# Performance work log

Hardware: AMD Instinct MI355X
Metric: run time of the kernel (lower is better)

## Reference

```python
import jax, jax.numpy as jnp
import numpy as np

DIM = 64
D_STATE = 64          # = d_inner // 2, required for consistency
D_CONV = 4
EXPAND = 2
D_INNER = EXPAND * DIM  # 128
BATCH = 2
SEQ = 2048


def setup_inputs() -> dict:
    key = jax.random.key(0)
    k0, k1, k2, k3, k4, k5 = jax.random.split(key, 6)
    return {
        "x": jax.random.normal(k0, (BATCH, SEQ, DIM), jnp.float32),
        # torch nn.Linear weight layout: (out_features, in_features)
        "W_proj": jax.random.normal(k1, (3 * D_INNER, DIM), jnp.float32) / np.sqrt(DIM),
        # torch depthwise Conv1d weight layout: (d_inner, 1, d_conv)
        "conv_w": jax.random.normal(k2, (D_INNER, 1, D_CONV), jnp.float32) / np.sqrt(D_CONV),
        "conv_b": jax.random.normal(k3, (D_INNER,), jnp.float32) * 0.01,
        # negative A so exp(delta * rowsum(A)) is a stable decay (<1)
        "A": -jnp.abs(jax.random.normal(k4, (D_STATE, D_STATE), jnp.float32)) * 0.1,
        "D": jax.random.normal(k5, (D_INNER,), jnp.float32),
    }


def _scan_dir(A_bar, bx, reverse):
    # A_bar, bx: (B, L, n, d). Linear recurrence h_t = A_t * h_{t-1} + bx_t.
    A_t = jnp.moveaxis(A_bar, 1, 0)  # (L, B, n, d)
    b_t = jnp.moveaxis(bx, 1, 0)
    h0 = jnp.zeros(A_t.shape[1:], A_t.dtype)

    def step(h, inp):
        a, b = inp
        h = a * h + b
        return h, h

    _, hs = jax.lax.scan(step, h0, (A_t, b_t), reverse=reverse)
    return jnp.moveaxis(hs, 0, 1)  # (B, L, n, d)


def _forward(x, W_proj, conv_w, conv_b, A, D):
    d_inner = D.shape[0]
    n = A.shape[0]
    k = conv_w.shape[-1]

    xp = x @ W_proj.T                                   # (B, L, 3*d_inner)
    x_c_in, delta_raw, BC = jnp.split(xp, [d_inner, 2 * d_inner], axis=-1)

    # causal depthwise conv1d (torch pads d_conv-1 both sides then slices [:L])
    xc = jnp.swapaxes(x_c_in, 1, 2)                     # (B, d, L)
    xc = jax.lax.conv_general_dilated(
        xc, conv_w, window_strides=(1,), padding=[(k - 1, 0)],
        dimension_numbers=("NCH", "OIH", "NCH"), feature_group_count=d_inner)
    xc = xc + conv_b[None, :, None]
    x_conv = jnp.swapaxes(xc, 1, 2)                     # (B, L, d_inner)

    delta = jax.nn.sigmoid(delta_raw)                   # (B, L, d_inner)
    B_in, C_in = BC[..., :n], BC[..., n:]               # (B, L, n) each

    a = A.sum(axis=1)                                   # 'ij->i' contraction, (n,)
    # A_bar[b,l,n,d] = exp(delta[b,l,d] * a[n])
    A_bar = jnp.exp(delta[:, :, None, :] * a[None, None, :, None])
    # (delta*B) * x, broadcast into (B, L, n, d)
    bx = (delta * x_conv)[:, :, None, :] * B_in[..., None]

    h = _scan_dir(A_bar, bx, False) + _scan_dir(A_bar, bx, True)  # (B,L,n,d)

    y = jnp.einsum("blnd,bln->bld", h, C_in) + D * x_conv
    return y


def reference(x, W_proj, conv_w, conv_b, A, D):
    return _forward(x, W_proj, conv_w, conv_b, A, D)
```

## Files before the change

### kernel.cpp

```cpp
#include <hip/hip_runtime.h>

#define BB   2
#define TT   2048
#define DIN  128
#define NS   64
#define CL   16
#define NC   128
#define NSUP 16
#define SUPW 8
#define NP   32
#define L2E  1.4426950408889634f

typedef float f2_t __attribute__((ext_vector_type(2)));
typedef float f4_t __attribute__((ext_vector_type(4)));

#if __has_builtin(__builtin_amdgcn_exp2f)
__device__ __forceinline__ float fexp2(float x) { return __builtin_amdgcn_exp2f(x); }
#else
__device__ __forceinline__ float fexp2(float x) { return exp2f(x); }
#endif

__device__ __forceinline__ unsigned int f2bfu(float f) {
  unsigned int u = __float_as_uint(f);
  u += 0x7FFFu + ((u >> 16) & 1u);
  return u >> 16;
}
__device__ __forceinline__ unsigned int packbf2(float a, float b) {
  return f2bfu(a) | (f2bfu(b) << 16);
}
__device__ __forceinline__ float bflo(unsigned int u) { return __uint_as_float(u << 16); }
__device__ __forceinline__ float bfhi(unsigned int u) { return __uint_as_float(u & 0xFFFF0000u); }

__global__ __launch_bounds__(128) void k_proj(
    const float* __restrict__ x, const float* __restrict__ W,
    const float* __restrict__ A,
    float* __restrict__ xcin, float* __restrict__ delta,
    float* __restrict__ Bb, float* __restrict__ Cb, float* __restrict__ a2g) {
  __shared__ float xs[128 * 65];
  int tile = blockIdx.x, rg = blockIdx.y, tid = threadIdx.x;
  int base = tile * 128;
  const float4* __restrict__ x4 = (const float4*)(x + (size_t)base * 64);
  for (int i = tid; i < 128 * 16; i += 128) {
    float4 v = x4[i];
    int row = i >> 4, c4 = (i & 15) << 2;
    xs[row * 65 + c4 + 0] = v.x;
    xs[row * 65 + c4 + 1] = v.y;
    xs[row * 65 + c4 + 2] = v.z;
    xs[row * 65 + c4 + 3] = v.w;
  }
  if (tile == 0 && rg == 0 && tid < NS) {
    float s = 0.f;
    for (int m = 0; m < NS; ++m) s += A[tid * NS + m];
    a2g[tid] = s * L2E;
  }
  __syncthreads();
  float xr[64];
#pragma unroll
  for (int k = 0; k < 64; ++k) xr[k] = xs[tid * 65 + k];
  int bt = base + tid;
#pragma unroll 4
  for (int rr = 0; rr < 16; ++rr) {
    int r = rg * 16 + rr;
    const float* __restrict__ wrow = W + r * 64;
    float a0 = 0.f, a1 = 0.f, a2 = 0.f, a3 = 0.f;
#pragma unroll
    for (int k = 0; k < 64; k += 4) {
      a0 = fmaf(xr[k + 0], wrow[k + 0], a0);
      a1 = fmaf(xr[k + 1], wrow[k + 1], a1);
      a2 = fmaf(xr[k + 2], wrow[k + 2], a2);
      a3 = fmaf(xr[k + 3], wrow[k + 3], a3);
    }
    float acc = (a0 + a1) + (a2 + a3);
    if (r < 128) {
      xcin[(size_t)bt * DIN + r] = acc;
    } else if (r < 256) {
      delta[(size_t)bt * DIN + (r - 128)] = 1.f / (1.f + fexp2(-acc * L2E));
    } else if (r < 320) {
      Bb[(size_t)bt * NS + (r - 256)] = acc;
    } else {
      Cb[(size_t)bt * NS + (r - 320)] = acc;
    }
  }
}

__global__ __launch_bounds__(1024) void k_scan1(
    const float* __restrict__ xcin, const float* __restrict__ delta,
    const float* __restrict__ Bb, const float* __restrict__ a2g,
    const float* __restrict__ cw, const float* __restrict__ cb,
    unsigned int* __restrict__ hendP, float* __restrict__ sumd) {
  __shared__ float xcs[(CL + 3) * DIN];
  __shared__ float des[CL * DIN];
  __shared__ float Bs[CL * NS];
  int c = blockIdx.x, b = blockIdx.y;
  int tid = threadIdx.x;
  int d = tid & 127;
  int g = __builtin_amdgcn_readfirstlane(tid >> 7);
  int t0 = c * CL;
  {
    const float* __restrict__ xcB = xcin + (size_t)b * TT * DIN;
    for (int i = tid; i < (CL + 3) * 32; i += 1024) {
      int row = i >> 5, c4 = i & 31;
      int t = t0 - 3 + row;
      float4 v = make_float4(0.f, 0.f, 0.f, 0.f);
      if (t >= 0) v = ((const float4*)(xcB + (size_t)t * DIN))[c4];
      ((float4*)xcs)[i] = v;
    }
    if (tid < CL * 32)
      ((float4*)des)[tid] = ((const float4*)(delta + (size_t)(b * TT + t0) * DIN))[tid];
    if (tid < CL * 16)
      ((float4*)Bs)[tid] = ((const float4*)(Bb + (size_t)(b * TT + t0) * NS))[tid];
  }
  float cw0 = cw[d * 4 + 0], cw1 = cw[d * 4 + 1], cw2 = cw[d * 4 + 2], cw3 = cw[d * 4 + 3];
  float cbd = cb[d];
  int nb = g * 8;
  f2_t a2p[4];
#pragma unroll
  for (int j = 0; j < 4; ++j) { a2p[j].x = a2g[nb + 2 * j]; a2p[j].y = a2g[nb + 2 * j + 1]; }
  __syncthreads();
  f2_t hf[4], hr[4], Pp[4];
#pragma unroll
  for (int j = 0; j < 4; ++j) {
    hf[j] = (f2_t){0.f, 0.f}; hr[j] = (f2_t){0.f, 0.f}; Pp[j] = (f2_t){1.f, 1.f};
  }
  float sd = 0.f;
  float w0 = xcs[0 * DIN + d], w1 = xcs[1 * DIN + d], w2 = xcs[2 * DIN + d];
#pragma unroll
  for (int i = 0; i < CL; ++i) {
    float w3 = xcs[(i + 3) * DIN + d];
    float xconv = fmaf(cw0, w0, fmaf(cw1, w1, fmaf(cw2, w2, fmaf(cw3, w3, cbd))));
    float de = des[i * DIN + d];
    sd += de;
    float dxv = de * xconv;
    const f2_t* __restrict__ B2 = (const f2_t*)&Bs[i * NS + nb];
#pragma unroll
    for (int j = 0; j < 4; ++j) {
      f2_t b2 = dxv * B2[j];
      f2_t e2;
      e2.x = fexp2(de * a2p[j].x);
      e2.y = fexp2(de * a2p[j].y);
      hf[j] = e2 * hf[j] + b2;
      hr[j] = Pp[j] * b2 + hr[j];
      Pp[j] = Pp[j] * e2;
    }
    w0 = w1; w1 = w2; w2 = w3;
  }
  size_t h0 = (((size_t)(0 * NC + c) * BB + b) * NP + (nb >> 1)) * DIN + d;
  size_t h1 = (((size_t)(1 * NC + c) * BB + b) * NP + (nb >> 1)) * DIN + d;
#pragma unroll
  for (int j = 0; j < 4; ++j) {
    hendP[h0 + (size_t)j * DIN] = packbf2(hf[j].x, hf[j].y);
    hendP[h1 + (size_t)j * DIN] = packbf2(hr[j].x, hr[j].y);
  }
  if (g == 0) sumd[(c * BB + b) * DIN + d] = sd;
}

__global__ __launch_bounds__(512) void k_comb(
    const unsigned int* __restrict__ hendP, const float* __restrict__ sumd,
    const float* __restrict__ a2g, unsigned int* __restrict__ hinP) {
  __shared__ float S0[NSUP][64], S1[NSUP][64];
  __shared__ float sdS[NSUP][64];
  __shared__ float C0[NSUP][64], C1[NSUP][64];
  int bid = blockIdx.x;
  int dh = bid & 1;
  int np = (bid >> 1) & 31;
  int dir = (bid >> 6) & 1;
  int b = bid >> 7;
  int tid = threadIdx.x;
  int dl = tid & 63;
  int d = dh * 64 + dl;
  int sl = __builtin_amdgcn_readfirstlane(tid >> 6);
  float a2n0 = a2g[2 * np], a2n1 = a2g[2 * np + 1];
  float hinLo0[2][SUPW], hinLo1[2][SUPW], pfLoc[2][SUPW];
#pragma unroll
  for (int ss = 0; ss < 2; ++ss) {
    int sp = sl + ss * 8;
    float c0 = 0.f, c1 = 0.f, pf = 0.f;
#pragma unroll
    for (int k = 0; k < SUPW; ++k) {
      int cc = sp * SUPW + (dir ? (SUPW - 1 - k) : k);
      float sdv = sumd[(cc * BB + b) * DIN + d];
      unsigned int hv = hendP[(((size_t)(dir * NC + cc) * BB + b) * NP + np) * DIN + d];
      hinLo0[ss][k] = c0; hinLo1[ss][k] = c1; pfLoc[ss][k] = pf;
      float e0 = fexp2(a2n0 * sdv);
      float e1 = fexp2(a2n1 * sdv);
      c0 = fmaf(e0, c0, bflo(hv));
      c1 = fmaf(e1, c1, bfhi(hv));
      pf += sdv;
    }
    S0[sp][dl] = c0; S1[sp][dl] = c1; sdS[sp][dl] = pf;
  }
  __syncthreads();
  if (sl == 0) {
    float c0 = 0.f, c1 = 0.f;
#pragma unroll
    for (int k = 0; k < NSUP; ++k) {
      int sp = dir ? (NSUP - 1 - k) : k;
      C0[sp][dl] = c0; C1[sp][dl] = c1;
      float sv = sdS[sp][dl];
      float e0 = fexp2(a2n0 * sv);
      float e1 = fexp2(a2n1 * sv);
      c0 = fmaf(e0, c0, S0[sp][dl]);
      c1 = fmaf(e1, c1, S1[sp][dl]);
    }
  }
  __syncthreads();
#pragma unroll
  for (int ss = 0; ss < 2; ++ss) {
    int sp = sl + ss * 8;
    float cs0 = C0[sp][dl], cs1 = C1[sp][dl];
#pragma unroll
    for (int k = 0; k < SUPW; ++k) {
      int cc = sp * SUPW + (dir ? (SUPW - 1 - k) : k);
      float pe0 = fexp2(a2n0 * pfLoc[ss][k]);
      float pe1 = fexp2(a2n1 * pfLoc[ss][k]);
      float v0 = fmaf(pe0, cs0, hinLo0[ss][k]);
      float v1 = fmaf(pe1, cs1, hinLo1[ss][k]);
      hinP[(((size_t)(dir * NC + cc) * BB + b) * NP + np) * DIN + d] = packbf2(v0, v1);
    }
  }
}

__global__ __launch_bounds__(1024) void k_scan2(
    const float* __restrict__ xcin, const float* __restrict__ delta,
    const float* __restrict__ Bb, const float* __restrict__ Cb,
    const float* __restrict__ a2g, const float* __restrict__ cw,
    const float* __restrict__ cb, const float* __restrict__ Dp,
    const unsigned int* __restrict__ hinP,
    float* __restrict__ out) {
  __shared__ float yred[8][CL][DIN];
  int c = blockIdx.x, b = blockIdx.y;
  int tid = threadIdx.x;
  int d = tid & 127;
  int g = __builtin_amdgcn_readfirstlane(tid >> 7);
  int dir = g >> 2;
  int nb = (g & 3) * 16;
  float cw0 = cw[d * 4 + 0], cw1 = cw[d * 4 + 1], cw2 = cw[d * 4 + 2], cw3 = cw[d * 4 + 3];
  float cbd = cb[d];
  float Dd = Dp[d];
  f2_t a2p[8];
#pragma unroll
  for (int j = 0; j < 8; ++j) { a2p[j].x = a2g[nb + 2 * j]; a2p[j].y = a2g[nb + 2 * j + 1]; }
  f2_t h2[8];
  size_t hb0 = (((size_t)(dir * NC + c) * BB + b) * NP + (nb >> 1)) * DIN + d;
#pragma unroll
  for (int jp = 0; jp < 8; ++jp) {
    unsigned int u = hinP[hb0 + (size_t)jp * DIN];
    h2[jp].x = bflo(u);
    h2[jp].y = bfhi(u);
  }
  int t0 = c * CL;
  const float* __restrict__ xcB = xcin + (size_t)b * TT * DIN + d;
  const float* __restrict__ deB = delta + (size_t)b * TT * DIN + d;
  const float* __restrict__ BbB = Bb + (size_t)b * TT * NS + nb;
  const float* __restrict__ CbB = Cb + (size_t)b * TT * NS + nb;
  bool addD = (g == 0);
  float w0, w1, w2, w3;
  if (dir == 0) {
    int t = t0;
    w0 = (t - 3 >= 0) ? xcB[(t - 3) * DIN] : 0.f;
    w1 = (t - 2 >= 0) ? xcB[(t - 2) * DIN] : 0.f;
    w2 = (t - 1 >= 0) ? xcB[(t - 1) * DIN] : 0.f;
    w3 = xcB[t * DIN];
#pragma unroll
    for (int i = 0; i < CL; ++i) {
      float xconv = fmaf(cw0, w0, fmaf(cw1, w1, fmaf(cw2, w2, fmaf(cw3, w3, cbd))));
      float de = deB[t * DIN];
      float dxv = de * xconv;
      f2_t y2 = (f2_t){0.f, 0.f};
#pragma unroll
      for (int jq = 0; jq < 4; ++jq) {
        f4_t bq = *(const f4_t*)&BbB[t * NS + jq * 4];
        f4_t cq = *(const f4_t*)&CbB[t * NS + jq * 4];
        f2_t blo = __builtin_shufflevector(bq, bq, 0, 1);
        f2_t bhi = __builtin_shufflevector(bq, bq, 2, 3);
        f2_t clo = __builtin_shufflevector(cq, cq, 0, 1);
        f2_t chi = __builtin_shufflevector(cq, cq, 2, 3);
        int jp = 2 * jq;
        f2_t e2;
        e2.x = fexp2(de * a2p[jp].x);
        e2.y = fexp2(de * a2p[jp].y);
        h2[jp] = e2 * h2[jp] + dxv * blo;
        y2 = h2[jp] * clo + y2;
        f2_t e3;
        e3.x = fexp2(de * a2p[jp + 1].x);
        e3.y = fexp2(de * a2p[jp + 1].y);
        h2[jp + 1] = e3 * h2[jp + 1] + dxv * bhi;
        y2 = h2[jp + 1] * chi + y2;
      }
      float yv = y2.x + y2.y;
      if (addD) yv = fmaf(Dd, xconv, yv);
      yred[g][i][d] = yv;
      if (i < CL - 1) { ++t; w0 = w1; w1 = w2; w2 = w3; w3 = xcB[t * DIN]; }
    }
  } else {
    int t = t0 + CL - 1;
    w3 = xcB[t * DIN];
    w2 = xcB[(t - 1) * DIN];
    w1 = xcB[(t - 2) * DIN];
    w0 = xcB[(t - 3) * DIN];
#pragma unroll
    for (int i = 0; i < CL; ++i) {
      float xconv = fmaf(cw0, w0, fmaf(cw1, w1, fmaf(cw2, w2, fmaf(cw3, w3, cbd))));
      float de = deB[t * DIN];
      float dxv = de * xconv;
      f2_t y2 = (f2_t){0.f, 0.f};
#pragma unroll
      for (int jq = 0; jq < 4; ++jq) {
        f4_t bq = *(const f4_t*)&BbB[t * NS + jq * 4];
        f4_t cq = *(const f4_t*)&CbB[t * NS + jq * 4];
        f2_t blo = __builtin_shufflevector(bq, bq, 0, 1);
        f2_t bhi = __builtin_shufflevector(bq, bq, 2, 3);
        f2_t clo = __builtin_shufflevector(cq, cq, 0, 1);
        f2_t chi = __builtin_shufflevector(cq, cq, 2, 3);
        int jp = 2 * jq;
        f2_t e2;
        e2.x = fexp2(de * a2p[jp].x);
        e2.y = fexp2(de * a2p[jp].y);
        h2[jp] = e2 * h2[jp] + dxv * blo;
        y2 = h2[jp] * clo + y2;
        f2_t e3;
        e3.x = fexp2(de * a2p[jp + 1].x);
        e3.y = fexp2(de * a2p[jp + 1].y);
        h2[jp + 1] = e3 * h2[jp + 1] + dxv * bhi;
        y2 = h2[jp + 1] * chi + y2;
      }
      float yv = y2.x + y2.y;
      yred[g][i][d] = yv;
      if (i < CL - 1) { --t; w3 = w2; w2 = w1; w1 = w0; w0 = (t - 3 >= 0) ? xcB[(t - 3) * DIN] : 0.f; }
    }
  }
  __syncthreads();
#pragma unroll
  for (int k = 0; k < 2; ++k) {
    int p = k * 1024 + tid;
    int i = p >> 7, d2 = p & 127;
    int ir = CL - 1 - i;
    float sf = (yred[0][i][d2] + yred[1][i][d2]) + (yred[2][i][d2] + yred[3][i][d2]);
    float sr = (yred[4][ir][d2] + yred[5][ir][d2]) + (yred[6][ir][d2] + yred[7][ir][d2]);
    out[((size_t)b * TT + t0 + i) * DIN + d2] = sf + sr;
  }
}

extern "C" void kernel_launch(void* const* d_in, const int* in_sizes, int n_in,
                              void* d_out, int out_size, void* d_ws, size_t ws_size,
                              hipStream_t stream) {
  const float* x  = (const float*)d_in[0];
  const float* W  = (const float*)d_in[1];
  const float* cw = (const float*)d_in[2];
  const float* cb = (const float*)d_in[3];
  const float* A  = (const float*)d_in[4];
  const float* Dp = (const float*)d_in[5];
  float* out = (float*)d_out;

  float* ws = (float*)d_ws;
  float* xcin   = ws;
  float* delta  = xcin + 524288;
  float* Bbuf   = delta + 524288;
  float* Cbuf   = Bbuf + 262144;
  float* a2g    = Cbuf + 262144;
  float* sumd   = a2g + 128;
  unsigned int* hendP = (unsigned int*)(sumd + 32768);
  unsigned int* hinP  = hendP + 2097152;

  hipLaunchKernelGGL(k_proj,  dim3(32, 24), dim3(128), 0, stream,
                     x, W, A, xcin, delta, Bbuf, Cbuf, a2g);
  hipLaunchKernelGGL(k_scan1, dim3(NC, BB), dim3(1024), 0, stream,
                     xcin, delta, Bbuf, a2g, cw, cb, hendP, sumd);
  hipLaunchKernelGGL(k_comb,  dim3(256), dim3(512), 0, stream,
                     hendP, sumd, a2g, hinP);
  hipLaunchKernelGGL(k_scan2, dim3(NC, BB), dim3(1024), 0, stream,
                     xcin, delta, Bbuf, Cbuf, a2g, cw, cb, Dp, hinP, out);
}
```

Measured before the change: 57.11 us.

## Precompute delta*xconv and D*xconv in scan1, interleave buffers for scan2

The first scan kernel now writes delta*xconv and D*xconv into workspace. This lets the second scan skip recomputing the causal conv and its sliding-window loads of xcin. Delta and dx are interleaved per timestep, as are B and C, so each timestep's operands sit in contiguous rows. The cost is extra global writes in scan1 and an extra ybase read in the output reduction.

```diff
diff --git a/kernel.cpp b/kernel.cpp
--- a/kernel.cpp
+++ b/kernel.cpp
@@ -34,8 +34,8 @@
 __global__ __launch_bounds__(128) void k_proj(
     const float* __restrict__ x, const float* __restrict__ W,
     const float* __restrict__ A,
-    float* __restrict__ xcin, float* __restrict__ delta,
-    float* __restrict__ Bb, float* __restrict__ Cb, float* __restrict__ a2g) {
+    float* __restrict__ xcin, float* __restrict__ ddx,
+    float* __restrict__ BC, float* __restrict__ a2g) {
   __shared__ float xs[128 * 65];
   int tile = blockIdx.x, rg = blockIdx.y, tid = threadIdx.x;
   int base = tile * 128;
@@ -50,7 +50,8 @@
   }
   if (tile == 0 && rg == 0 && tid < NS) {
     float s = 0.f;
-    for (int m = 0; m < NS; ++m) s += A[tid * NS + m];
+    const float* __restrict__ Ar = A + tid * NS;
+    for (int m = 0; m < NS; ++m) s += Ar[m];
     a2g[tid] = s * L2E;
   }
   __syncthreads();
@@ -74,19 +75,20 @@
     if (r < 128) {
       xcin[(size_t)bt * DIN + r] = acc;
     } else if (r < 256) {
-      delta[(size_t)bt * DIN + (r - 128)] = 1.f / (1.f + fexp2(-acc * L2E));
+      ddx[(size_t)bt * 256 + (r - 128)] = 1.f / (1.f + fexp2(-acc * L2E));
     } else if (r < 320) {
-      Bb[(size_t)bt * NS + (r - 256)] = acc;
+      BC[(size_t)bt * 128 + (r - 256)] = acc;
     } else {
-      Cb[(size_t)bt * NS + (r - 320)] = acc;
+      BC[(size_t)bt * 128 + 64 + (r - 320)] = acc;
     }
   }
 }
 
 __global__ __launch_bounds__(1024) void k_scan1(
-    const float* __restrict__ xcin, const float* __restrict__ delta,
-    const float* __restrict__ Bb, const float* __restrict__ a2g,
+    const float* __restrict__ xcin, float* __restrict__ ddx,
+    const float* __restrict__ BC, const float* __restrict__ a2g,
     const float* __restrict__ cw, const float* __restrict__ cb,
+    const float* __restrict__ Dp, float* __restrict__ ybase,
     unsigned int* __restrict__ hendP, float* __restrict__ sumd) {
   __shared__ float xcs[(CL + 3) * DIN];
   __shared__ float des[CL * DIN];
@@ -105,13 +107,20 @@
       if (t >= 0) v = ((const float4*)(xcB + (size_t)t * DIN))[c4];
       ((float4*)xcs)[i] = v;
     }
-    if (tid < CL * 32)
-      ((float4*)des)[tid] = ((const float4*)(delta + (size_t)(b * TT + t0) * DIN))[tid];
-    if (tid < CL * 16)
-      ((float4*)Bs)[tid] = ((const float4*)(Bb + (size_t)(b * TT + t0) * NS))[tid];
+    if (tid < CL * 32) {
+      int row = tid >> 5, c4 = tid & 31;
+      ((float4*)des)[tid] =
+          ((const float4*)(ddx + (size_t)(b * TT + t0 + row) * 256))[c4];
+    }
+    if (tid < CL * 16) {
+      int row = tid >> 4, c4 = tid & 15;
+      ((float4*)Bs)[tid] =
+          ((const float4*)(BC + (size_t)(b * TT + t0 + row) * 128))[c4];
+    }
   }
   float cw0 = cw[d * 4 + 0], cw1 = cw[d * 4 + 1], cw2 = cw[d * 4 + 2], cw3 = cw[d * 4 + 3];
   float cbd = cb[d];
+  float Dd = Dp[d];
   int nb = g * 8;
   f2_t a2p[4];
 #pragma unroll
@@ -124,6 +133,8 @@
   }
   float sd = 0.f;
   float w0 = xcs[0 * DIN + d], w1 = xcs[1 * DIN + d], w2 = xcs[2 * DIN + d];
+  float* __restrict__ dxB = ddx + (size_t)(b * TT + t0) * 256 + 128 + d;
+  float* __restrict__ ybB = ybase + (size_t)(b * TT + t0) * DIN + d;
 #pragma unroll
   for (int i = 0; i < CL; ++i) {
     float w3 = xcs[(i + 3) * DIN + d];
@@ -131,6 +142,10 @@
     float de = des[i * DIN + d];
     sd += de;
     float dxv = de * xconv;
+    if (g == 0) {
+      dxB[i * 256] = dxv;
+      ybB[i * DIN] = Dd * xconv;
+    }
     const f2_t* __restrict__ B2 = (const f2_t*)&Bs[i * NS + nb];
 #pragma unroll
     for (int j = 0; j < 4; ++j) {
@@ -221,10 +236,8 @@
 }
 
 __global__ __launch_bounds__(1024) void k_scan2(
-    const float* __restrict__ xcin, const float* __restrict__ delta,
-    const float* __restrict__ Bb, const float* __restrict__ Cb,
-    const float* __restrict__ a2g, const float* __restrict__ cw,
-    const float* __restrict__ cb, const float* __restrict__ Dp,
+    const float* __restrict__ ddx, const float* __restrict__ BC,
+    const float* __restrict__ a2g, const float* __restrict__ ybase,
     const unsigned int* __restrict__ hinP,
     float* __restrict__ out) {
   __shared__ float yred[8][CL][DIN];
@@ -234,9 +247,6 @@
   int g = __builtin_amdgcn_readfirstlane(tid >> 7);
   int dir = g >> 2;
   int nb = (g & 3) * 16;
-  float cw0 = cw[d * 4 + 0], cw1 = cw[d * 4 + 1], cw2 = cw[d * 4 + 2], cw3 = cw[d * 4 + 3];
-  float cbd = cb[d];
-  float Dd = Dp[d];
   f2_t a2p[8];
 #pragma unroll
   for (int j = 0; j < 8; ++j) { a2p[j].x = a2g[nb + 2 * j]; a2p[j].y = a2g[nb + 2 * j + 1]; }
@@ -249,28 +259,18 @@
     h2[jp].y = bfhi(u);
   }
   int t0 = c * CL;
-  const float* __restrict__ xcB = xcin + (size_t)b * TT * DIN + d;
-  const float* __restrict__ deB = delta + (size_t)b * TT * DIN + d;
-  const float* __restrict__ BbB = Bb + (size_t)b * TT * NS + nb;
-  const float* __restrict__ CbB = Cb + (size_t)b * TT * NS + nb;
-  bool addD = (g == 0);
-  float w0, w1, w2, w3;
+  const float* __restrict__ ddB = ddx + (size_t)(b * TT + t0) * 256 + d;
+  const float* __restrict__ BCB = BC + (size_t)(b * TT + t0) * 128 + nb;
   if (dir == 0) {
-    int t = t0;
-    w0 = (t - 3 >= 0) ? xcB[(t - 3) * DIN] : 0.f;
-    w1 = (t - 2 >= 0) ? xcB[(t - 2) * DIN] : 0.f;
-    w2 = (t - 1 >= 0) ? xcB[(t - 1) * DIN] : 0.f;
-    w3 = xcB[t * DIN];
 #pragma unroll
     for (int i = 0; i < CL; ++i) {
-      float xconv = fmaf(cw0, w0, fmaf(cw1, w1, fmaf(cw2, w2, fmaf(cw3, w3, cbd))));
-      float de = deB[t * DIN];
-      float dxv = de * xconv;
+      float de  = ddB[i * 256];
+      float dxv = ddB[i * 256 + 128];
       f2_t y2 = (f2_t){0.f, 0.f};
 #pragma unroll
       for (int jq = 0; jq < 4; ++jq) {
-        f4_t bq = *(const f4_t*)&BbB[t * NS + jq * 4];
-        f4_t cq = *(const f4_t*)&CbB[t * NS + jq * 4];
+        f4_t bq = *(const f4_t*)&BCB[i * 128 + jq * 4];
+        f4_t cq = *(const f4_t*)&BCB[i * 128 + 64 + jq * 4];
         f2_t blo = __builtin_shufflevector(bq, bq, 0, 1);
         f2_t bhi = __builtin_shufflevector(bq, bq, 2, 3);
         f2_t clo = __builtin_shufflevector(cq, cq, 0, 1);
@@ -287,27 +287,19 @@
         h2[jp + 1] = e3 * h2[jp + 1] + dxv * bhi;
         y2 = h2[jp + 1] * chi + y2;
       }
-      float yv = y2.x + y2.y;
-      if (addD) yv = fmaf(Dd, xconv, yv);
-      yred[g][i][d] = yv;
-      if (i < CL - 1) { ++t; w0 = w1; w1 = w2; w2 = w3; w3 = xcB[t * DIN]; }
+      yred[g][i][d] = y2.x + y2.y;
     }
   } else {
-    int t = t0 + CL - 1;
-    w3 = xcB[t * DIN];
-    w2 = xcB[(t - 1) * DIN];
-    w1 = xcB[(t - 2) * DIN];
-    w0 = xcB[(t - 3) * DIN];
 #pragma unroll
     for (int i = 0; i < CL; ++i) {
-      float xconv = fmaf(cw0, w0, fmaf(cw1, w1, fmaf(cw2, w2, fmaf(cw3, w3, cbd))));
-      float de = deB[t * DIN];
-      float dxv = de * xconv;
+      int ti = CL - 1 - i;
+      float de  = ddB[ti * 256];
+      float dxv = ddB[ti * 256 + 128];
       f2_t y2 = (f2_t){0.f, 0.f};
 #pragma unroll
       for (int jq = 0; jq < 4; ++jq) {
-        f4_t bq = *(const f4_t*)&BbB[t * NS + jq * 4];
-        f4_t cq = *(const f4_t*)&CbB[t * NS + jq * 4];
+        f4_t bq = *(const f4_t*)&BCB[ti * 128 + jq * 4];
+        f4_t cq = *(const f4_t*)&BCB[ti * 128 + 64 + jq * 4];
         f2_t blo = __builtin_shufflevector(bq, bq, 0, 1);
         f2_t bhi = __builtin_shufflevector(bq, bq, 2, 3);
         f2_t clo = __builtin_shufflevector(cq, cq, 0, 1);
@@ -324,9 +316,7 @@
         h2[jp + 1] = e3 * h2[jp + 1] + dxv * bhi;
         y2 = h2[jp + 1] * chi + y2;
       }
-      float yv = y2.x + y2.y;
-      yred[g][i][d] = yv;
-      if (i < CL - 1) { --t; w3 = w2; w2 = w1; w1 = w0; w0 = (t - 3 >= 0) ? xcB[(t - 3) * DIN] : 0.f; }
+      yred[g][i][d] = y2.x + y2.y;
     }
   }
   __syncthreads();
@@ -337,7 +327,8 @@
     int ir = CL - 1 - i;
     float sf = (yred[0][i][d2] + yred[1][i][d2]) + (yred[2][i][d2] + yred[3][i][d2]);
     float sr = (yred[4][ir][d2] + yred[5][ir][d2]) + (yred[6][ir][d2] + yred[7][ir][d2]);
-    out[((size_t)b * TT + t0 + i) * DIN + d2] = sf + sr;
+    size_t oidx = ((size_t)b * TT + t0 + i) * DIN + d2;
+    out[oidx] = sf + sr + ybase[oidx];
   }
 }
 
@@ -354,20 +345,20 @@
 
   float* ws = (float*)d_ws;
   float* xcin   = ws;
-  float* delta  = xcin + 524288;
-  float* Bbuf   = delta + 524288;
-  float* Cbuf   = Bbuf + 262144;
-  float* a2g    = Cbuf + 262144;
+  float* ddx    = xcin + 524288;
+  float* BCbuf  = ddx + 1048576;
+  float* ybase  = BCbuf + 524288;
+  float* a2g    = ybase + 524288;
   float* sumd   = a2g + 128;
   unsigned int* hendP = (unsigned int*)(sumd + 32768);
   unsigned int* hinP  = hendP + 2097152;
 
   hipLaunchKernelGGL(k_proj,  dim3(32, 24), dim3(128), 0, stream,
-                     x, W, A, xcin, delta, Bbuf, Cbuf, a2g);
+                     x, W, A, xcin, ddx, BCbuf, a2g);
   hipLaunchKernelGGL(k_scan1, dim3(NC, BB), dim3(1024), 0, stream,
-                     xcin, delta, Bbuf, a2g, cw, cb, hendP, sumd);
+                     xcin, ddx, BCbuf, a2g, cw, cb, Dp, ybase, hendP, sumd);
   hipLaunchKernelGGL(k_comb,  dim3(256), dim3(512), 0, stream,
                      hendP, sumd, a2g, hinP);
   hipLaunchKernelGGL(k_scan2, dim3(NC, BB), dim3(1024), 0, stream,
-                     xcin, delta, Bbuf, Cbuf, a2g, cw, cb, Dp, hinP, out);
-}
+                     ddx, BCbuf, a2g, ybase, hinP, out);
+}
```

After: 64.78 us. +13.4%, slower.
